# Performance work log

Measured on AMD Instinct MI355X. Metric: run time of the kernel, lower is better.

## Reference

```python
import jax, jax.numpy as jnp
import numpy as np

D_IN = 1024
D_OUT = 1024
SEQ = 2048
BATCH = 4


def setup_inputs() -> dict:
    key = jax.random.key(0)
    k_x, k_q, k_k, k_v = jax.random.split(key, 4)
    scale = 1.0 / np.sqrt(D_IN)  # ~ torch Linear init scale
    x = jax.random.normal(k_x, (BATCH, SEQ, D_IN), dtype=jnp.float32)
    # torch nn.Linear weights have shape [d_out, d_in]; y = x @ W.T
    Wq = jax.random.uniform(k_q, (D_OUT, D_IN), jnp.float32, -scale, scale)
    Wk = jax.random.uniform(k_k, (D_OUT, D_IN), jnp.float32, -scale, scale)
    Wv = jax.random.uniform(k_v, (D_OUT, D_IN), jnp.float32, -scale, scale)
    return {"x": x, "Wq": Wq, "Wk": Wk, "Wv": Wv}


def reference(x, Wq, Wk, Wv):
    # projections (no bias, qkv_bias=False)
    q = jnp.einsum("bsd,ed->bse", x, Wq)  # [B,S,D_OUT]
    k = jnp.einsum("bsd,ed->bse", x, Wk)
    v = jnp.einsum("bsd,ed->bse", x, Wv)
    scores = jnp.einsum("bqe,bke->bqk", q, k)  # [B,S,S]
    seq = scores.shape[-1]
    causal = jnp.tril(jnp.ones((seq, seq), dtype=bool))  # keep lower-tri
    scores = jnp.where(causal[None], scores, -jnp.inf)
    # note: original scales AFTER masking: softmax(scores / sqrt(d_k))
    inv_sqrt_dk = 1.0 / np.sqrt(k.shape[-1]).astype(np.float32)
    weights = jax.nn.softmax(scores * inv_sqrt_dk, axis=-1)
    # dropout p=0.0 (eval-equivalent): identity
    return jnp.einsum("bqk,bke->bqe", weights, v)
```

## Files before the change

kernel.cpp:

```cpp
#include <hip/hip_runtime.h>
#include <hip/hip_bf16.h>

typedef __bf16 v8bf __attribute__((ext_vector_type(8)));
typedef float v4f __attribute__((ext_vector_type(4)));

#define GBL_AS(p) ((const __attribute__((address_space(1))) unsigned int*)(p))
#define LDS_AS(p) ((__attribute__((address_space(3))) unsigned int*)(p))

#define WAIT_VM4() __builtin_amdgcn_s_waitcnt(0x0F74)
#define WAIT_VM6() __builtin_amdgcn_s_waitcnt(0x0F76)
#define WAIT_VM0() __builtin_amdgcn_s_waitcnt(0x0F70)

__global__ void cast_f32_bf16(const float* __restrict__ src,
                              __hip_bfloat16* __restrict__ dst, int n) {
  int i = (blockIdx.x * 256 + threadIdx.x) * 4;
  if (i >= n) return;
  float4 f = *(const float4*)(src + i);
  union { __hip_bfloat16 h[4]; uint2 u; } pk;
  pk.h[0] = __float2bfloat16(f.x);
  pk.h[1] = __float2bfloat16(f.y);
  pk.h[2] = __float2bfloat16(f.z);
  pk.h[3] = __float2bfloat16(f.w);
  *(uint2*)(dst + i) = pk.u;
}

__global__ void cast_w3(const float* __restrict__ a, const float* __restrict__ b,
                        const float* __restrict__ c, __hip_bfloat16* __restrict__ dst) {
  int seg = blockIdx.x >> 10;
  const float* src = seg == 0 ? a : (seg == 1 ? b : c);
  int i = ((blockIdx.x & 1023) * 256 + threadIdx.x) * 4;
  float4 f = *(const float4*)(src + i);
  union { __hip_bfloat16 h[4]; uint2 u; } pk;
  pk.h[0] = __float2bfloat16(f.x);
  pk.h[1] = __float2bfloat16(f.y);
  pk.h[2] = __float2bfloat16(f.z);
  pk.h[3] = __float2bfloat16(f.w);
  *(uint2*)(dst + seg * 1048576 + i) = pk.u;
}

template<int MODE>
__device__ static __forceinline__
void gemm_nt_body(const __hip_bfloat16* __restrict__ A, long sAb, int lda,
                  const __hip_bfloat16* __restrict__ B, long sBb, int ldb,
                  void* __restrict__ Cv, long sCb, int ldc,
                  int K, float scale, float* __restrict__ sums) {
  const int tid = threadIdx.x;
  const int l = tid & 63, w = tid >> 6;
  int z, nb, mb, kend = K;
  if (MODE == 1) {
    const int id = blockIdx.x;
    z = id & 3;
    const int t = id >> 2;
    int m = (int)((__builtin_sqrtf(8.0f * t + 1.0f) - 1.0f) * 0.5f);
    while ((m + 1) * (m + 2) / 2 <= t) ++m;
    while (m * (m + 1) / 2 > t) --m;
    mb = m << 7;
    nb = (t - m * (m + 1) / 2) << 7;
  } else {
    const int id = blockIdx.x;
    const int half = id >> 8, r8 = id & 255;
    const int m = r8 >> 4, low = r8 & 15;
    nb = (low >> 1) << 7;
    z = (half << 1) | (low & 1);
    const int mi = half ? (15 - m) : m;
    mb = mi << 7;
    kend = (mi + 1) << 7;
  }

  A += (long)z * sAb;
  B += (long)z * sBb;

  __shared__ alignas(16) __hip_bfloat16 As[3][128 * 32];
  __shared__ alignas(16) __hip_bfloat16 Bs[3][128 * 32];

  v4f acc[4][4] = {};
  const int wm = (w >> 1) * 64, wn = (w & 1) * 64;

  const int cb0 = w * 64;
  const int q0 = cb0 + l, r0s = q0 >> 2;
  const int c0s = ((q0 & 3) ^ ((r0s >> 1) & 3)) << 3;
  const int cb1 = 256 + w * 64;
  const int q1 = cb1 + l, r1s = q1 >> 2;
  const int c1s = ((q1 & 3) ^ ((r1s >> 1) & 3)) << 3;

  const __hip_bfloat16* Arow0 = A + (long)(mb + r0s) * lda + c0s;
  const __hip_bfloat16* Arow1 = A + (long)(mb + r1s) * lda + c1s;
  const __hip_bfloat16* Brow0 = B + (long)(nb + r0s) * ldb + c0s;
  const __hip_bfloat16* Brow1 = B + (long)(nb + r1s) * ldb + c1s;

  const int arow = wm + (l & 15);
  const int ldsA = arow * 32 + ((((l >> 4) ^ ((arow >> 1) & 3))) << 3);
  const int brow = wn + (l & 15);
  const int ldsB = brow * 32 + ((((l >> 4) ^ ((brow >> 1) & 3))) << 3);

#define STAGE_T(K0, BUF) do {                                                   \
    __builtin_amdgcn_global_load_lds(GBL_AS(Arow0 + (K0)),                      \
        LDS_AS(&As[BUF][cb0 * 8]), 16, 0, 0);                                   \
    __builtin_amdgcn_global_load_lds(GBL_AS(Brow0 + (K0)),                      \
        LDS_AS(&Bs[BUF][cb0 * 8]), 16, 0, 0);                                   \
    __builtin_amdgcn_global_load_lds(GBL_AS(Arow1 + (K0)),                      \
        LDS_AS(&As[BUF][cb1 * 8]), 16, 0, 0);                                   \
    __builtin_amdgcn_global_load_lds(GBL_AS(Brow1 + (K0)),                      \
        LDS_AS(&Bs[BUF][cb1 * 8]), 16, 0, 0);                                   \
  } while (0)

#define COMPUTE(BI) do {                                                        \
    v8bf af[4], bfr[4];                                                         \
    _Pragma("unroll")                                                           \
    for (int i = 0; i < 4; ++i) {                                               \
      af[i]  = *(const v8bf*)(&As[BI][ldsA + i * 512]);                         \
      bfr[i] = *(const v8bf*)(&Bs[BI][ldsB + i * 512]);                         \
    }                                                                           \
    _Pragma("unroll")                                                           \
    for (int i = 0; i < 4; ++i)                                                 \
      _Pragma("unroll")                                                         \
      for (int j = 0; j < 4; ++j)                                               \
        acc[i][j] = __builtin_amdgcn_mfma_f32_16x16x32_bf16(af[i], bfr[j],      \
                                                            acc[i][j], 0, 0, 0);\
  } while (0)

#define KITER(IT) do {                                                          \
    if constexpr ((IT) < 31) WAIT_VM4(); else WAIT_VM0();                       \
    __builtin_amdgcn_s_barrier();                                               \
    if constexpr ((IT) < 30) STAGE_T((IT) * 32 + 64, ((IT) + 2) % 3);           \
    COMPUTE((IT) % 3);                                                          \
  } while (0)

  if constexpr (MODE == 1) {
    STAGE_T(0, 0);
    STAGE_T(32, 1);
    KITER(0);  KITER(1);  KITER(2);  KITER(3);  KITER(4);  KITER(5);  KITER(6);
    KITER(7);  KITER(8);  KITER(9);  KITER(10); KITER(11); KITER(12); KITER(13);
    KITER(14); KITER(15); KITER(16); KITER(17); KITER(18); KITER(19); KITER(20);
    KITER(21); KITER(22); KITER(23); KITER(24); KITER(25); KITER(26); KITER(27);
    KITER(28); KITER(29); KITER(30); KITER(31);
  } else {
    auto stage = [&](int k0, int buf) {
      __builtin_amdgcn_global_load_lds(GBL_AS(Arow0 + k0),
          LDS_AS(&As[buf][cb0 * 8]), 16, 0, 0);
      __builtin_amdgcn_global_load_lds(GBL_AS(Brow0 + k0),
          LDS_AS(&Bs[buf][cb0 * 8]), 16, 0, 0);
      __builtin_amdgcn_global_load_lds(GBL_AS(Arow1 + k0),
          LDS_AS(&As[buf][cb1 * 8]), 16, 0, 0);
      __builtin_amdgcn_global_load_lds(GBL_AS(Brow1 + k0),
          LDS_AS(&Bs[buf][cb1 * 8]), 16, 0, 0);
    };
    stage(0, 0);
    if (32 < kend) stage(32, 1);
    int bi = 0;
    for (int k0 = 0; k0 < kend; k0 += 32) {
      if (k0 + 32 < kend) WAIT_VM4(); else WAIT_VM0();
      __builtin_amdgcn_s_barrier();
      if (k0 + 64 < kend) stage(k0 + 64, bi == 0 ? 2 : bi - 1);
      v8bf af[4], bfr[4];
#pragma unroll
      for (int i = 0; i < 4; ++i) {
        af[i]  = *(const v8bf*)(&As[bi][ldsA + i * 512]);
        bfr[i] = *(const v8bf*)(&Bs[bi][ldsB + i * 512]);
      }
#pragma unroll
      for (int i = 0; i < 4; ++i)
#pragma unroll
        for (int j = 0; j < 4; ++j)
          acc[i][j] = __builtin_amdgcn_mfma_f32_16x16x32_bf16(af[i], bfr[j], acc[i][j], 0, 0, 0);
      bi = (bi == 2) ? 0 : bi + 1;
    }
  }
#undef KITER
#undef COMPUTE
#undef STAGE_T

  const int col0 = nb + wn + (l & 15);
  const int row0 = mb + wm + ((l >> 4) << 2);
  if constexpr (MODE == 1) {
    __hip_bfloat16* C = (__hip_bfloat16*)Cv + (long)z * sCb;
    float* srow = sums + z * 2048;
#pragma unroll
    for (int i = 0; i < 4; ++i)
#pragma unroll
      for (int r = 0; r < 4; ++r) {
        const int m = row0 + i * 16 + r;
        long ro = (long)m * ldc;
        float sp = 0.f;
#pragma unroll
        for (int j = 0; j < 4; ++j) {
          const int n = col0 + j * 16;
          float p = (n <= m) ? __expf(acc[i][j][r] * scale) : 0.0f;
          sp += p;
          C[ro + n] = __float2bfloat16(p);
        }
        sp += __shfl_xor(sp, 1);
        sp += __shfl_xor(sp, 2);
        sp += __shfl_xor(sp, 4);
        sp += __shfl_xor(sp, 8);
        if ((l & 15) == 0) atomicAdd(&srow[m], sp);
      }
  } else {
    float* C = (float*)Cv + (long)z * sCb;
    const float* srow = sums + z * 2048;
#pragma unroll
    for (int i = 0; i < 4; ++i)
#pragma unroll
      for (int r = 0; r < 4; ++r) {
        const int m = row0 + i * 16 + r;
        const float s = 1.0f / srow[m];
        long ro = (long)m * ldc;
#pragma unroll
        for (int j = 0; j < 4; ++j)
          C[ro + col0 + j * 16] = acc[i][j][r] * s;
      }
  }
}

__global__ __launch_bounds__(256, 3)
void gemm_score(const __hip_bfloat16* __restrict__ A, long sAb, int lda,
                const __hip_bfloat16* __restrict__ B, long sBb, int ldb,
                void* __restrict__ Cv, long sCb, int ldc,
                int K, float scale, float* __restrict__ sums) {
  gemm_nt_body<1>(A, sAb, lda, B, sBb, ldb, Cv, sCb, ldc, K, scale, sums);
}

__global__ __launch_bounds__(256, 3)
void gemm_pv(const __hip_bfloat16* __restrict__ A, long sAb, int lda,
             const __hip_bfloat16* __restrict__ B, long sBb, int ldb,
             void* __restrict__ Cv, long sCb, int ldc,
             int K, float scale, float* __restrict__ sums) {
  gemm_nt_body<2>(A, sAb, lda, B, sBb, ldb, Cv, sCb, ldc, K, scale, sums);
}

__global__ __launch_bounds__(256, 2)
void gemm_proj(const __hip_bfloat16* __restrict__ A, int lda,
               const __hip_bfloat16* __restrict__ B, long sBb, int ldb,
               __hip_bfloat16* __restrict__ C, long sCb, int ldc,
               float scale, __hip_bfloat16* __restrict__ vTp) {
  const int tid = threadIdx.x;
  const int l = tid & 63, w = tid >> 6;
  const int z  = blockIdx.x >> 3;
  const int nb = (blockIdx.x & 7) << 7;
  const int mb = blockIdx.y << 8;

  B += (long)z * sBb;

  __shared__ alignas(16) __hip_bfloat16 As[3][256 * 32];
  __shared__ alignas(16) __hip_bfloat16 Bs[3][128 * 32];

  v4f acc[8][4] = {};
  const int wm = (w >> 1) << 7;
  const int wn = (w & 1) << 6;

  const int qa0 = 0 * 256 + w * 64 + l, ra0 = qa0 >> 2;
  const int qa1 = 1 * 256 + w * 64 + l, ra1 = qa1 >> 2;
  const int qa2 = 2 * 256 + w * 64 + l, ra2 = qa2 >> 2;
  const int qa3 = 3 * 256 + w * 64 + l, ra3 = qa3 >> 2;
  const __hip_bfloat16* sA0 = A + (long)(mb + ra0) * lda + (((qa0 & 3) ^ ((ra0 >> 1) & 3)) << 3);
  const __hip_bfloat16* sA1 = A + (long)(mb + ra1) * lda + (((qa1 & 3) ^ ((ra1 >> 1) & 3)) << 3);
  const __hip_bfloat16* sA2 = A + (long)(mb + ra2) * lda + (((qa2 & 3) ^ ((ra2 >> 1) & 3)) << 3);
  const __hip_bfloat16* sA3 = A + (long)(mb + ra3) * lda + (((qa3 & 3) ^ ((ra3 >> 1) & 3)) << 3);
  const int qb0 = 0 * 256 + w * 64 + l, rb0 = qb0 >> 2;
  const int qb1 = 1 * 256 + w * 64 + l, rb1 = qb1 >> 2;
  const __hip_bfloat16* sB0 = B + (long)(nb + rb0) * ldb + (((qb0 & 3) ^ ((rb0 >> 1) & 3)) << 3);
  const __hip_bfloat16* sB1 = B + (long)(nb + rb1) * ldb + (((qb1 & 3) ^ ((rb1 >> 1) & 3)) << 3);

  const int arow = wm + (l & 15);
  const int ldsA = arow * 32 + ((((l >> 4) ^ ((arow >> 1) & 3))) << 3);
  const int brow = wn + (l & 15);
  const int ldsB = brow * 32 + ((((l >> 4) ^ ((brow >> 1) & 3))) << 3);

#define STAGE_P(K0, BUF) do {                                                   \
    __builtin_amdgcn_global_load_lds(GBL_AS(sA0 + (K0)),                        \
        LDS_AS(&As[BUF][0 * 2048 + w * 512]), 16, 0, 0);                        \
    __builtin_amdgcn_global_load_lds(GBL_AS(sA1 + (K0)),                        \
        LDS_AS(&As[BUF][1 * 2048 + w * 512]), 16, 0, 0);                        \
    __builtin_amdgcn_global_load_lds(GBL_AS(sA2 + (K0)),                        \
        LDS_AS(&As[BUF][2 * 2048 + w * 512]), 16, 0, 0);                        \
    __builtin_amdgcn_global_load_lds(GBL_AS(sA3 + (K0)),                        \
        LDS_AS(&As[BUF][3 * 2048 + w * 512]), 16, 0, 0);                        \
    __builtin_amdgcn_global_load_lds(GBL_AS(sB0 + (K0)),                        \
        LDS_AS(&Bs[BUF][0 * 2048 + w * 512]), 16, 0, 0);                        \
    __builtin_amdgcn_global_load_lds(GBL_AS(sB1 + (K0)),                        \
        LDS_AS(&Bs[BUF][1 * 2048 + w * 512]), 16, 0, 0);                        \
  } while (0)

#define COMPUTE_P(BI) do {                                                      \
    v8bf af[8], bfr[4];                                                         \
    _Pragma("unroll")                                                           \
    for (int i = 0; i < 8; ++i)                                                 \
      af[i]  = *(const v8bf*)(&As[BI][ldsA + i * 512]);                         \
    _Pragma("unroll")                                                           \
    for (int j = 0; j < 4; ++j)                                                 \
      bfr[j] = *(const v8bf*)(&Bs[BI][ldsB + j * 512]);                         \
    _Pragma("unroll")                                                           \
    for (int i = 0; i < 8; ++i)                                                 \
      _Pragma("unroll")                                                         \
      for (int j = 0; j < 4; ++j)                                               \
        acc[i][j] = __builtin_amdgcn_mfma_f32_16x16x32_bf16(af[i], bfr[j],      \
                                                            acc[i][j], 0, 0, 0);\
  } while (0)

#define KITER_P(IT) do {                                                        \
    if constexpr ((IT) < 31) WAIT_VM6(); else WAIT_VM0();                       \
    __builtin_amdgcn_s_barrier();                                               \
    if constexpr ((IT) < 30) STAGE_P((IT) * 32 + 64, ((IT) + 2) % 3);           \
    COMPUTE_P((IT) % 3);                                                        \
  } while (0)

  STAGE_P(0, 0);
  STAGE_P(32, 1);
  KITER_P(0);  KITER_P(1);  KITER_P(2);  KITER_P(3);  KITER_P(4);  KITER_P(5);
  KITER_P(6);  KITER_P(7);  KITER_P(8);  KITER_P(9);  KITER_P(10); KITER_P(11);
  KITER_P(12); KITER_P(13); KITER_P(14); KITER_P(15); KITER_P(16); KITER_P(17);
  KITER_P(18); KITER_P(19); KITER_P(20); KITER_P(21); KITER_P(22); KITER_P(23);
  KITER_P(24); KITER_P(25); KITER_P(26); KITER_P(27); KITER_P(28); KITER_P(29);
  KITER_P(30); KITER_P(31);
#undef KITER_P
#undef COMPUTE_P
#undef STAGE_P

  const int col0 = nb + wn + (l & 15);
  const int row0 = mb + wm + ((l >> 4) << 2);
  if (z < 2) {
    __hip_bfloat16* Cz = C + (long)z * sCb;
#pragma unroll
    for (int i = 0; i < 8; ++i)
#pragma unroll
      for (int r = 0; r < 4; ++r) {
        long ro = (long)(row0 + i * 16 + r) * ldc;
#pragma unroll
        for (int j = 0; j < 4; ++j)
          Cz[ro + col0 + j * 16] = __float2bfloat16(acc[i][j][r] * scale);
      }
  } else {
    const long b = row0 >> 11;
    const int seq0 = row0 & 2047;
#pragma unroll
    for (int i = 0; i < 8; ++i)
#pragma unroll
      for (int j = 0; j < 4; ++j) {
        union { __hip_bfloat16 h[4]; uint2 u; } pk;
#pragma unroll
        for (int r = 0; r < 4; ++r) pk.h[r] = __float2bfloat16(acc[i][j][r]);
        *(uint2*)(vTp + b * 2097152 + (long)(col0 + j * 16) * 2048 +
                  (seq0 + i * 16)) = pk.u;
      }
  }
}

extern "C" void kernel_launch(void* const* d_in, const int* in_sizes, int n_in,
                              void* d_out, int out_size, void* d_ws, size_t ws_size,
                              hipStream_t stream) {
  const float* x  = (const float*)d_in[0];
  const float* Wq = (const float*)d_in[1];
  const float* Wk = (const float*)d_in[2];
  const float* Wv = (const float*)d_in[3];
  float* out = (float*)d_out;
  char* ws = (char*)d_ws;

  __hip_bfloat16* qkv = (__hip_bfloat16*)ws;
  __hip_bfloat16* vT  = (__hip_bfloat16*)(ws + 50331648);
  __hip_bfloat16* xb  = (__hip_bfloat16*)(ws + 67108864);
  __hip_bfloat16* Wb  = (__hip_bfloat16*)(ws + 83886080);
  __hip_bfloat16* P   = (__hip_bfloat16*)(ws + 67108864);
  float* sums         = (float*)(ws + 100663296);

  hipMemsetAsync(sums, 0, 8192 * sizeof(float), stream);

  cast_f32_bf16<<<8192, 256, 0, stream>>>(x, xb, 8388608);
  cast_w3<<<3072, 256, 0, stream>>>(Wq, Wk, Wv, Wb);

  gemm_proj<<<dim3(24, 32, 1), 256, 0, stream>>>(
      xb, 1024, Wb, 1048576L, 1024, qkv, 8388608L, 1024, 1.0f, vT);

  gemm_score<<<dim3(544, 1, 1), 256, 0, stream>>>(
      qkv, 2097152L, 1024, qkv + 8388608, 2097152L, 1024,
      P, 4194304L, 2048, 1024, 0.03125f, sums);

  gemm_pv<<<dim3(512, 1, 1), 256, 0, stream>>>(
      P, 4194304L, 2048, vT, 2097152L, 2048,
      out, 2097152L, 1024, 2048, 1.0f, sums);
}
```

Baseline: 232.4 us.

## Split score GEMM into 64-row tiles and split-K long causal rows in PV

The score GEMM now uses 64x128 tiles over the causal triangle, giving 1088 blocks at higher occupancy instead of 544 blocks of 128x128. The PV GEMM splits the K range in half for the lower row tiles (m>=8), which have the longest causal K, and accumulates into pre-zeroed output with float atomics. This is meant to balance work across CUs and reduce tail imbalance. The cost is extra memsets, atomic traffic on half the output, and lower MFMA reuse per block in the score kernel.

```diff
diff --git a/kernel.cpp b/kernel.cpp
--- a/kernel.cpp
+++ b/kernel.cpp
@@ -7,8 +7,8 @@
 #define GBL_AS(p) ((const __attribute__((address_space(1))) unsigned int*)(p))
 #define LDS_AS(p) ((__attribute__((address_space(3))) unsigned int*)(p))
 
+#define WAIT_VM3() __builtin_amdgcn_s_waitcnt(0x0F73)
 #define WAIT_VM4() __builtin_amdgcn_s_waitcnt(0x0F74)
-#define WAIT_VM6() __builtin_amdgcn_s_waitcnt(0x0F76)
 #define WAIT_VM0() __builtin_amdgcn_s_waitcnt(0x0F70)
 
 __global__ void cast_f32_bf16(const float* __restrict__ src,
@@ -36,196 +36,6 @@
   pk.h[2] = __float2bfloat16(f.z);
   pk.h[3] = __float2bfloat16(f.w);
   *(uint2*)(dst + seg * 1048576 + i) = pk.u;
-}
-
-template<int MODE>
-__device__ static __forceinline__
-void gemm_nt_body(const __hip_bfloat16* __restrict__ A, long sAb, int lda,
-                  const __hip_bfloat16* __restrict__ B, long sBb, int ldb,
-                  void* __restrict__ Cv, long sCb, int ldc,
-                  int K, float scale, float* __restrict__ sums) {
-  const int tid = threadIdx.x;
-  const int l = tid & 63, w = tid >> 6;
-  int z, nb, mb, kend = K;
-  if (MODE == 1) {
-    const int id = blockIdx.x;
-    z = id & 3;
-    const int t = id >> 2;
-    int m = (int)((__builtin_sqrtf(8.0f * t + 1.0f) - 1.0f) * 0.5f);
-    while ((m + 1) * (m + 2) / 2 <= t) ++m;
-    while (m * (m + 1) / 2 > t) --m;
-    mb = m << 7;
-    nb = (t - m * (m + 1) / 2) << 7;
-  } else {
-    const int id = blockIdx.x;
-    const int half = id >> 8, r8 = id & 255;
-    const int m = r8 >> 4, low = r8 & 15;
-    nb = (low >> 1) << 7;
-    z = (half << 1) | (low & 1);
-    const int mi = half ? (15 - m) : m;
-    mb = mi << 7;
-    kend = (mi + 1) << 7;
-  }
-
-  A += (long)z * sAb;
-  B += (long)z * sBb;
-
-  __shared__ alignas(16) __hip_bfloat16 As[3][128 * 32];
-  __shared__ alignas(16) __hip_bfloat16 Bs[3][128 * 32];
-
-  v4f acc[4][4] = {};
-  const int wm = (w >> 1) * 64, wn = (w & 1) * 64;
-
-  const int cb0 = w * 64;
-  const int q0 = cb0 + l, r0s = q0 >> 2;
-  const int c0s = ((q0 & 3) ^ ((r0s >> 1) & 3)) << 3;
-  const int cb1 = 256 + w * 64;
-  const int q1 = cb1 + l, r1s = q1 >> 2;
-  const int c1s = ((q1 & 3) ^ ((r1s >> 1) & 3)) << 3;
-
-  const __hip_bfloat16* Arow0 = A + (long)(mb + r0s) * lda + c0s;
-  const __hip_bfloat16* Arow1 = A + (long)(mb + r1s) * lda + c1s;
-  const __hip_bfloat16* Brow0 = B + (long)(nb + r0s) * ldb + c0s;
-  const __hip_bfloat16* Brow1 = B + (long)(nb + r1s) * ldb + c1s;
-
-  const int arow = wm + (l & 15);
-  const int ldsA = arow * 32 + ((((l >> 4) ^ ((arow >> 1) & 3))) << 3);
-  const int brow = wn + (l & 15);
-  const int ldsB = brow * 32 + ((((l >> 4) ^ ((brow >> 1) & 3))) << 3);
-
-#define STAGE_T(K0, BUF) do {                                                   \
-    __builtin_amdgcn_global_load_lds(GBL_AS(Arow0 + (K0)),                      \
-        LDS_AS(&As[BUF][cb0 * 8]), 16, 0, 0);                                   \
-    __builtin_amdgcn_global_load_lds(GBL_AS(Brow0 + (K0)),                      \
-        LDS_AS(&Bs[BUF][cb0 * 8]), 16, 0, 0);                                   \
-    __builtin_amdgcn_global_load_lds(GBL_AS(Arow1 + (K0)),                      \
-        LDS_AS(&As[BUF][cb1 * 8]), 16, 0, 0);                                   \
-    __builtin_amdgcn_global_load_lds(GBL_AS(Brow1 + (K0)),                      \
-        LDS_AS(&Bs[BUF][cb1 * 8]), 16, 0, 0);                                   \
-  } while (0)
-
-#define COMPUTE(BI) do {                                                        \
-    v8bf af[4], bfr[4];                                                         \
-    _Pragma("unroll")                                                           \
-    for (int i = 0; i < 4; ++i) {                                               \
-      af[i]  = *(const v8bf*)(&As[BI][ldsA + i * 512]);                         \
-      bfr[i] = *(const v8bf*)(&Bs[BI][ldsB + i * 512]);                         \
-    }                                                                           \
-    _Pragma("unroll")                                                           \
-    for (int i = 0; i < 4; ++i)                                                 \
-      _Pragma("unroll")                                                         \
-      for (int j = 0; j < 4; ++j)                                               \
-        acc[i][j] = __builtin_amdgcn_mfma_f32_16x16x32_bf16(af[i], bfr[j],      \
-                                                            acc[i][j], 0, 0, 0);\
-  } while (0)
-
-#define KITER(IT) do {                                                          \
-    if constexpr ((IT) < 31) WAIT_VM4(); else WAIT_VM0();                       \
-    __builtin_amdgcn_s_barrier();                                               \
-    if constexpr ((IT) < 30) STAGE_T((IT) * 32 + 64, ((IT) + 2) % 3);           \
-    COMPUTE((IT) % 3);                                                          \
-  } while (0)
-
-  if constexpr (MODE == 1) {
-    STAGE_T(0, 0);
-    STAGE_T(32, 1);
-    KITER(0);  KITER(1);  KITER(2);  KITER(3);  KITER(4);  KITER(5);  KITER(6);
-    KITER(7);  KITER(8);  KITER(9);  KITER(10); KITER(11); KITER(12); KITER(13);
-    KITER(14); KITER(15); KITER(16); KITER(17); KITER(18); KITER(19); KITER(20);
-    KITER(21); KITER(22); KITER(23); KITER(24); KITER(25); KITER(26); KITER(27);
-    KITER(28); KITER(29); KITER(30); KITER(31);
-  } else {
-    auto stage = [&](int k0, int buf) {
-      __builtin_amdgcn_global_load_lds(GBL_AS(Arow0 + k0),
-          LDS_AS(&As[buf][cb0 * 8]), 16, 0, 0);
-      __builtin_amdgcn_global_load_lds(GBL_AS(Brow0 + k0),
-          LDS_AS(&Bs[buf][cb0 * 8]), 16, 0, 0);
-      __builtin_amdgcn_global_load_lds(GBL_AS(Arow1 + k0),
-          LDS_AS(&As[buf][cb1 * 8]), 16, 0, 0);
-      __builtin_amdgcn_global_load_lds(GBL_AS(Brow1 + k0),
-          LDS_AS(&Bs[buf][cb1 * 8]), 16, 0, 0);
-    };
-    stage(0, 0);
-    if (32 < kend) stage(32, 1);
-    int bi = 0;
-    for (int k0 = 0; k0 < kend; k0 += 32) {
-      if (k0 + 32 < kend) WAIT_VM4(); else WAIT_VM0();
-      __builtin_amdgcn_s_barrier();
-      if (k0 + 64 < kend) stage(k0 + 64, bi == 0 ? 2 : bi - 1);
-      v8bf af[4], bfr[4];
-#pragma unroll
-      for (int i = 0; i < 4; ++i) {
-        af[i]  = *(const v8bf*)(&As[bi][ldsA + i * 512]);
-        bfr[i] = *(const v8bf*)(&Bs[bi][ldsB + i * 512]);
-      }
-#pragma unroll
-      for (int i = 0; i < 4; ++i)
-#pragma unroll
-        for (int j = 0; j < 4; ++j)
-          acc[i][j] = __builtin_amdgcn_mfma_f32_16x16x32_bf16(af[i], bfr[j], acc[i][j], 0, 0, 0);
-      bi = (bi == 2) ? 0 : bi + 1;
-    }
-  }
-#undef KITER
-#undef COMPUTE
-#undef STAGE_T
-
-  const int col0 = nb + wn + (l & 15);
-  const int row0 = mb + wm + ((l >> 4) << 2);
-  if constexpr (MODE == 1) {
-    __hip_bfloat16* C = (__hip_bfloat16*)Cv + (long)z * sCb;
-    float* srow = sums + z * 2048;
-#pragma unroll
-    for (int i = 0; i < 4; ++i)
-#pragma unroll
-      for (int r = 0; r < 4; ++r) {
-        const int m = row0 + i * 16 + r;
-        long ro = (long)m * ldc;
-        float sp = 0.f;
-#pragma unroll
-        for (int j = 0; j < 4; ++j) {
-          const int n = col0 + j * 16;
-          float p = (n <= m) ? __expf(acc[i][j][r] * scale) : 0.0f;
-          sp += p;
-          C[ro + n] = __float2bfloat16(p);
-        }
-        sp += __shfl_xor(sp, 1);
-        sp += __shfl_xor(sp, 2);
-        sp += __shfl_xor(sp, 4);
-        sp += __shfl_xor(sp, 8);
-        if ((l & 15) == 0) atomicAdd(&srow[m], sp);
-      }
-  } else {
-    float* C = (float*)Cv + (long)z * sCb;
-    const float* srow = sums + z * 2048;
-#pragma unroll
-    for (int i = 0; i < 4; ++i)
-#pragma unroll
-      for (int r = 0; r < 4; ++r) {
-        const int m = row0 + i * 16 + r;
-        const float s = 1.0f / srow[m];
-        long ro = (long)m * ldc;
-#pragma unroll
-        for (int j = 0; j < 4; ++j)
-          C[ro + col0 + j * 16] = acc[i][j][r] * s;
-      }
-  }
-}
-
-__global__ __launch_bounds__(256, 3)
-void gemm_score(const __hip_bfloat16* __restrict__ A, long sAb, int lda,
-                const __hip_bfloat16* __restrict__ B, long sBb, int ldb,
-                void* __restrict__ Cv, long sCb, int ldc,
-                int K, float scale, float* __restrict__ sums) {
-  gemm_nt_body<1>(A, sAb, lda, B, sBb, ldb, Cv, sCb, ldc, K, scale, sums);
-}
-
-__global__ __launch_bounds__(256, 3)
-void gemm_pv(const __hip_bfloat16* __restrict__ A, long sAb, int lda,
-             const __hip_bfloat16* __restrict__ B, long sBb, int ldb,
-             void* __restrict__ Cv, long sCb, int ldc,
-             int K, float scale, float* __restrict__ sums) {
-  gemm_nt_body<2>(A, sAb, lda, B, sBb, ldb, Cv, sCb, ldc, K, scale, sums);
 }
 
 __global__ __launch_bounds__(256, 2)
@@ -297,8 +107,9 @@
                                                             acc[i][j], 0, 0, 0);\
   } while (0)
 
+#define WAIT_VM6_() __builtin_amdgcn_s_waitcnt(0x0F76)
 #define KITER_P(IT) do {                                                        \
-    if constexpr ((IT) < 31) WAIT_VM6(); else WAIT_VM0();                       \
+    if constexpr ((IT) < 31) WAIT_VM6_(); else WAIT_VM0();                      \
     __builtin_amdgcn_s_barrier();                                               \
     if constexpr ((IT) < 30) STAGE_P((IT) * 32 + 64, ((IT) + 2) % 3);           \
     COMPUTE_P((IT) % 3);                                                        \
@@ -345,6 +156,220 @@
   }
 }
 
+__global__ __launch_bounds__(256, 4)
+void gemm_score64(const __hip_bfloat16* __restrict__ A, long sAb,
+                  const __hip_bfloat16* __restrict__ B, long sBb,
+                  __hip_bfloat16* __restrict__ C, long sCb,
+                  float scale, float* __restrict__ sums) {
+  const int tid = threadIdx.x;
+  const int l = tid & 63, w = tid >> 6;
+  const int id = blockIdx.x;
+  const int z = id / 272;
+  const int t = id - z * 272;
+  int p = (int)((__builtin_sqrtf(4.0f * t + 1.0f) - 1.0f) * 0.5f);
+  while ((p + 1) * (p + 2) <= t) ++p;
+  while (p * (p + 1) > t) --p;
+  const int rem = t - p * (p + 1);
+  const int mm = 2 * p + (rem > p);
+  const int nn = (rem > p) ? rem - (p + 1) : rem;
+  const int mb = mm << 6, nb = nn << 7;
+
+  const __hip_bfloat16* Az = A + (long)z * sAb;
+  const __hip_bfloat16* Bz = B + (long)z * sBb;
+
+  __shared__ alignas(16) __hip_bfloat16 As[3][64 * 32];
+  __shared__ alignas(16) __hip_bfloat16 Bs[3][128 * 32];
+
+  v4f acc[4][2] = {};
+  const int wn = w << 5;
+
+  const int ras = tid >> 2;
+  const int cas = ((tid & 3) ^ ((ras >> 1) & 3)) << 3;
+  const __hip_bfloat16* Arow = Az + (long)(mb + ras) * 1024 + cas;
+  const int r0s = tid >> 2;
+  const int c0s = ((tid & 3) ^ ((r0s >> 1) & 3)) << 3;
+  const int q1 = 256 + tid, r1s = q1 >> 2;
+  const int c1s = ((q1 & 3) ^ ((r1s >> 1) & 3)) << 3;
+  const __hip_bfloat16* Brow0 = Bz + (long)(nb + r0s) * 1024 + c0s;
+  const __hip_bfloat16* Brow1 = Bz + (long)(nb + r1s) * 1024 + c1s;
+
+  const int arow = l & 15;
+  const int ldsA = arow * 32 + ((((l >> 4) ^ ((arow >> 1) & 3))) << 3);
+  const int brow = wn + (l & 15);
+  const int ldsB = brow * 32 + ((((l >> 4) ^ ((brow >> 1) & 3))) << 3);
+
+#define STAGE_S(K0, BUF) do {                                                   \
+    __builtin_amdgcn_global_load_lds(GBL_AS(Arow + (K0)),                       \
+        LDS_AS(&As[BUF][tid * 8]), 16, 0, 0);                                   \
+    __builtin_amdgcn_global_load_lds(GBL_AS(Brow0 + (K0)),                      \
+        LDS_AS(&Bs[BUF][tid * 8]), 16, 0, 0);                                   \
+    __builtin_amdgcn_global_load_lds(GBL_AS(Brow1 + (K0)),                      \
+        LDS_AS(&Bs[BUF][2048 + tid * 8]), 16, 0, 0);                            \
+  } while (0)
+
+#define COMPUTE_S(BI) do {                                                      \
+    v8bf af[4], bfr[2];                                                         \
+    _Pragma("unroll")                                                           \
+    for (int i = 0; i < 4; ++i)                                                 \
+      af[i]  = *(const v8bf*)(&As[BI][ldsA + i * 512]);                         \
+    _Pragma("unroll")                                                           \
+    for (int j = 0; j < 2; ++j)                                                 \
+      bfr[j] = *(const v8bf*)(&Bs[BI][ldsB + j * 512]);                         \
+    _Pragma("unroll")                                                           \
+    for (int i = 0; i < 4; ++i)                                                 \
+      _Pragma("unroll")                                                         \
+      for (int j = 0; j < 2; ++j)                                               \
+        acc[i][j] = __builtin_amdgcn_mfma_f32_16x16x32_bf16(af[i], bfr[j],      \
+                                                            acc[i][j], 0, 0, 0);\
+  } while (0)
+
+#define KITER_S(IT) do {                                                        \
+    if constexpr ((IT) < 31) WAIT_VM3(); else WAIT_VM0();                       \
+    __builtin_amdgcn_s_barrier();                                               \
+    if constexpr ((IT) < 30) STAGE_S((IT) * 32 + 64, ((IT) + 2) % 3);           \
+    COMPUTE_S((IT) % 3);                                                        \
+  } while (0)
+
+  STAGE_S(0, 0);
+  STAGE_S(32, 1);
+  KITER_S(0);  KITER_S(1);  KITER_S(2);  KITER_S(3);  KITER_S(4);  KITER_S(5);
+  KITER_S(6);  KITER_S(7);  KITER_S(8);  KITER_S(9);  KITER_S(10); KITER_S(11);
+  KITER_S(12); KITER_S(13); KITER_S(14); KITER_S(15); KITER_S(16); KITER_S(17);
+  KITER_S(18); KITER_S(19); KITER_S(20); KITER_S(21); KITER_S(22); KITER_S(23);
+  KITER_S(24); KITER_S(25); KITER_S(26); KITER_S(27); KITER_S(28); KITER_S(29);
+  KITER_S(30); KITER_S(31);
+#undef KITER_S
+#undef COMPUTE_S
+#undef STAGE_S
+
+  __hip_bfloat16* Cz = C + (long)z * sCb;
+  float* srow = sums + z * 2048;
+  const int col0 = nb + wn + (l & 15);
+  const int row0 = mb + ((l >> 4) << 2);
+#pragma unroll
+  for (int i = 0; i < 4; ++i)
+#pragma unroll
+    for (int r = 0; r < 4; ++r) {
+      const int m = row0 + i * 16 + r;
+      const long ro = (long)m * 2048;
+      float sp = 0.f;
+#pragma unroll
+      for (int j = 0; j < 2; ++j) {
+        const int n = col0 + j * 16;
+        float pv = (n <= m) ? __expf(acc[i][j][r] * scale) : 0.0f;
+        sp += pv;
+        Cz[ro + n] = __float2bfloat16(pv);
+      }
+      sp += __shfl_xor(sp, 1);
+      sp += __shfl_xor(sp, 2);
+      sp += __shfl_xor(sp, 4);
+      sp += __shfl_xor(sp, 8);
+      if ((l & 15) == 0) atomicAdd(&srow[m], sp);
+    }
+}
+
+__global__ __launch_bounds__(256, 3)
+void gemm_pv(const __hip_bfloat16* __restrict__ A, long sAb, int lda,
+             const __hip_bfloat16* __restrict__ B, long sBb, int ldb,
+             float* __restrict__ C, long sCb, int ldc,
+             const float* __restrict__ sums) {
+  const int tid = threadIdx.x;
+  const int l = tid & 63, w = tid >> 6;
+  const int id = blockIdx.x;
+  const int z = id / 192;
+  const int rem = id - z * 192;
+  const int nn = rem / 24, s = rem - nn * 24;
+  int m, k0s, klen;
+  bool atom;
+  if (s < 8) {
+    m = s; k0s = 0; klen = (m + 1) << 7; atom = false;
+  } else {
+    const int u = s - 8;
+    m = 8 + (u >> 1);
+    const int h = ((m + 1) >> 1) << 7;
+    if (u & 1) { k0s = h; klen = ((m + 1) << 7) - h; }
+    else       { k0s = 0; klen = h; }
+    atom = true;
+  }
+  const int mb = m << 7, nb = nn << 7;
+
+  A += (long)z * sAb + k0s;
+  B += (long)z * sBb + k0s;
+
+  __shared__ alignas(16) __hip_bfloat16 As[3][128 * 32];
+  __shared__ alignas(16) __hip_bfloat16 Bs[3][128 * 32];
+
+  v4f acc[4][4] = {};
+  const int wm = (w >> 1) * 64, wn = (w & 1) * 64;
+
+  const int cb0 = w * 64;
+  const int q0 = cb0 + l, r0s = q0 >> 2;
+  const int c0s = ((q0 & 3) ^ ((r0s >> 1) & 3)) << 3;
+  const int cb1 = 256 + w * 64;
+  const int q1 = cb1 + l, r1s = q1 >> 2;
+  const int c1s = ((q1 & 3) ^ ((r1s >> 1) & 3)) << 3;
+
+  const __hip_bfloat16* Arow0 = A + (long)(mb + r0s) * lda + c0s;
+  const __hip_bfloat16* Arow1 = A + (long)(mb + r1s) * lda + c1s;
+  const __hip_bfloat16* Brow0 = B + (long)(nb + r0s) * ldb + c0s;
+  const __hip_bfloat16* Brow1 = B + (long)(nb + r1s) * ldb + c1s;
+
+  const int arow = wm + (l & 15);
+  const int ldsA = arow * 32 + ((((l >> 4) ^ ((arow >> 1) & 3))) << 3);
+  const int brow = wn + (l & 15);
+  const int ldsB = brow * 32 + ((((l >> 4) ^ ((brow >> 1) & 3))) << 3);
+
+  auto stage = [&](int k0, int buf) {
+    __builtin_amdgcn_global_load_lds(GBL_AS(Arow0 + k0),
+        LDS_AS(&As[buf][cb0 * 8]), 16, 0, 0);
+    __builtin_amdgcn_global_load_lds(GBL_AS(Brow0 + k0),
+        LDS_AS(&Bs[buf][cb0 * 8]), 16, 0, 0);
+    __builtin_amdgcn_global_load_lds(GBL_AS(Arow1 + k0),
+        LDS_AS(&As[buf][cb1 * 8]), 16, 0, 0);
+    __builtin_amdgcn_global_load_lds(GBL_AS(Brow1 + k0),
+        LDS_AS(&Bs[buf][cb1 * 8]), 16, 0, 0);
+  };
+  stage(0, 0);
+  if (32 < klen) stage(32, 1);
+  int bi = 0;
+  for (int k0 = 0; k0 < klen; k0 += 32) {
+    if (k0 + 32 < klen) WAIT_VM4(); else WAIT_VM0();
+    __builtin_amdgcn_s_barrier();
+    if (k0 + 64 < klen) stage(k0 + 64, bi == 0 ? 2 : bi - 1);
+    v8bf af[4], bfr[4];
+#pragma unroll
+    for (int i = 0; i < 4; ++i) {
+      af[i]  = *(const v8bf*)(&As[bi][ldsA + i * 512]);
+      bfr[i] = *(const v8bf*)(&Bs[bi][ldsB + i * 512]);
+    }
+#pragma unroll
+    for (int i = 0; i < 4; ++i)
+#pragma unroll
+      for (int j = 0; j < 4; ++j)
+        acc[i][j] = __builtin_amdgcn_mfma_f32_16x16x32_bf16(af[i], bfr[j], acc[i][j], 0, 0, 0);
+    bi = (bi == 2) ? 0 : bi + 1;
+  }
+
+  float* Cz = C + (long)z * sCb;
+  const float* srow = sums + z * 2048;
+  const int col0 = nb + wn + (l & 15);
+  const int row0 = mb + wm + ((l >> 4) << 2);
+#pragma unroll
+  for (int i = 0; i < 4; ++i)
+#pragma unroll
+    for (int r = 0; r < 4; ++r) {
+      const int mr = row0 + i * 16 + r;
+      const float sc = 1.0f / srow[mr];
+      const long ro = (long)mr * ldc;
+#pragma unroll
+      for (int j = 0; j < 4; ++j) {
+        const float v = acc[i][j][r] * sc;
+        if (atom) atomicAdd(&Cz[ro + col0 + j * 16], v);
+        else Cz[ro + col0 + j * 16] = v;
+      }
+    }
+}
+
 extern "C" void kernel_launch(void* const* d_in, const int* in_sizes, int n_in,
                               void* d_out, int out_size, void* d_ws, size_t ws_size,
                               hipStream_t stream) {
@@ -363,6 +388,8 @@
   float* sums         = (float*)(ws + 100663296);
 
   hipMemsetAsync(sums, 0, 8192 * sizeof(float), stream);
+  for (int z = 0; z < 4; ++z)
+    hipMemsetAsync(out + (long)z * 2097152 + 1048576, 0, 4194304, stream);
 
   cast_f32_bf16<<<8192, 256, 0, stream>>>(x, xb, 8388608);
   cast_w3<<<3072, 256, 0, stream>>>(Wq, Wk, Wv, Wb);
@@ -370,11 +397,11 @@
   gemm_proj<<<dim3(24, 32, 1), 256, 0, stream>>>(
       xb, 1024, Wb, 1048576L, 1024, qkv, 8388608L, 1024, 1.0f, vT);
 
-  gemm_score<<<dim3(544, 1, 1), 256, 0, stream>>>(
-      qkv, 2097152L, 1024, qkv + 8388608, 2097152L, 1024,
-      P, 4194304L, 2048, 1024, 0.03125f, sums);
-
-  gemm_pv<<<dim3(512, 1, 1), 256, 0, stream>>>(
+  gemm_score64<<<dim3(1088, 1, 1), 256, 0, stream>>>(
+      qkv, 2097152L, qkv + 8388608, 2097152L,
+      P, 4194304L, 0.03125f, sums);
+
+  gemm_pv<<<dim3(768, 1, 1), 256, 0, stream>>>(
       P, 4194304L, 2048, vT, 2097152L, 2048,
-      out, 2097152L, 1024, 2048, 1.0f, sums);
-}
+      out, 2097152L, 1024, sums);
+}
```

Result: slower. 267.1 us (+14.9%).
